# Kernel optimization log

Measured on AMD Instinct MI355X. Metric: run time of the kernel, lower is better.

## Reference

```python
import jax, jax.numpy as jnp
import numpy as np

B, C_IN, C_OUT, T, K, STRIDE, PAD = 16, 256, 256, 4096, 3, 1, 1


def deform_conv1d(x, offset, weight, bias):
    # x: (B,C,T); offset: (B,2K,Tout,1) interleaved (dy,dx); weight: (O,C,K); bias: (O,)
    Bn, C, Tn = x.shape
    O, _, Kn = weight.shape
    dy = offset[:, 0::2, :, 0]  # (B,K,Tout)
    dx = offset[:, 1::2, :, 0]  # (B,K,Tout)
    Tout = dy.shape[-1]
    # offset_mode='center': subtract dcn_base_offset (y base = k-pad, x base = 0)
    base_y = jnp.arange(Kn, dtype=x.dtype) - PAD
    dy = dy - base_y[None, :, None]
    # sampling position along T: t*stride - pad + k + dy
    t0 = jnp.arange(Tout, dtype=x.dtype) * STRIDE - PAD
    py = t0[None, None, :] + jnp.arange(Kn, dtype=x.dtype)[None, :, None] + dy  # (B,K,Tout)
    i0 = jnp.floor(py)
    frac = py - i0
    i0i = i0.astype(jnp.int32)

    def gather(idx):
        valid = ((idx >= 0) & (idx < Tn)).astype(x.dtype)  # zero padding outside
        idxc = jnp.clip(idx, 0, Tn - 1).reshape(Bn, 1, Kn * Tout)
        v = jnp.take_along_axis(x, jnp.broadcast_to(idxc, (Bn, C, Kn * Tout)), axis=2)
        return v.reshape(Bn, C, Kn, Tout) * valid[:, None]

    # linear interp along T
    v = gather(i0i) * (1.0 - frac)[:, None] + gather(i0i + 1) * frac[:, None]  # (B,C,K,Tout)
    # bilinear weight along the dummy width dim (W=1, base x index 0)
    wx = jnp.maximum(0.0, 1.0 - jnp.abs(dx))  # (B,K,Tout)
    v = v * wx[:, None]
    out = jnp.einsum('bckt,ock->bot', v, weight) + bias[None, :, None]
    return out


def setup_inputs() -> dict:
    key = jax.random.key(0)
    k1, k2, k3, k4 = jax.random.split(key, 4)
    x = jax.random.normal(k1, (B, C_IN, T), dtype=jnp.float32)
    offset = jax.random.normal(k2, (B, 2 * K, T, 1), dtype=jnp.float32)
    fan_in = C_IN * K
    bound = 1.0 / np.sqrt(fan_in)
    weight = jax.random.uniform(k3, (C_OUT, C_IN, K), minval=-bound, maxval=bound, dtype=jnp.float32)
    bias = jax.random.uniform(k4, (C_OUT,), minval=-bound, maxval=bound, dtype=jnp.float32)
    return {"x": x, "offset": offset, "weight": weight, "bias": bias}


def reference(x, offset, weight, bias):
    return deform_conv1d(x, offset, weight, bias)
```

## Files before the change

kernel.cpp:

```cpp
#include <hip/hip_runtime.h>
#include <hip/hip_bf16.h>

typedef __attribute__((ext_vector_type(8))) short bf16x8;
typedef __attribute__((ext_vector_type(4))) float f32x4;

constexpr int NB = 16, CIN = 256, COUT = 256, TDIM = 4096, KS = 3, PADV = 1;
constexpr int TT = 64;
constexpr int NSTEP = 12;

typedef __attribute__((address_space(1))) const unsigned int gu32;
typedef __attribute__((address_space(3))) unsigned int lu32;

static __device__ __forceinline__ ushort f2bf(float f) {
    union { __hip_bfloat16 h; ushort u; } cv;
    cv.h = __float2bfloat16(f);
    return cv.u;
}
static __device__ __forceinline__ float bf2f(ushort u) {
    union { unsigned int u32; float f; } cv;
    cv.u32 = ((unsigned int)u) << 16;
    return cv.f;
}

__global__ __launch_bounds__(256) void prepack_w2(const float* __restrict__ w,
                                                  __hip_bfloat16* __restrict__ wp2) {
    int idx = blockIdx.x * 256 + threadIdx.x;
    if (idx >= NSTEP * COUT * 64) return;
    int e    = idx & 7;
    int lane = (idx >> 3) & 63;
    int mf   = (idx >> 9) & 1;
    int kb   = (idx >> 10) & 1;
    int wid  = (idx >> 11) & 3;
    int ot   = (idx >> 13) & 1;
    int s    = idx >> 14;
    int o = ot * 128 + wid * 32 + mf * 16 + (lane & 15);
    int k = s % 3;
    int c = (s / 3) * 64 + kb * 32 + (lane >> 4) * 8 + e;
    wp2[idx] = __float2bfloat16(w[(o * CIN + c) * KS + k]);
}

__global__ __launch_bounds__(256) void prepack_w(const float* __restrict__ w,
                                                 __hip_bfloat16* __restrict__ wp) {
    int idx = blockIdx.x * 256 + threadIdx.x;
    if (idx >= NSTEP * COUT * 64) return;
    int e  = idx & 7;
    int j  = (idx >> 3) & 7;
    int o  = (idx >> 6) & (COUT - 1);
    int s  = idx >> 14;
    int k  = s % 3;
    int c  = (s / 3) * 64 + ((j ^ (o & 7)) << 3) + e;
    wp[idx] = __float2bfloat16(w[(o * CIN + c) * KS + k]);
}

__global__ __launch_bounds__(256) void transpose_x(const float* __restrict__ x,
                                                   ushort* __restrict__ xT) {
    __shared__ ushort tile[64][72];
    const int b  = blockIdx.z;
    const int c0 = blockIdx.y * 64;
    const int t0 = blockIdx.x * 64;
    const int tid = threadIdx.x;
    {
        const int c  = tid >> 2;
        const int tq = (tid & 3) << 4;
        const float* src = x + ((size_t)(b * CIN + c0 + c)) * TDIM + t0 + tq;
        #pragma unroll
        for (int i = 0; i < 4; ++i) {
            float4 f = *(const float4*)(src + 4 * i);
            tile[tq + 4 * i + 0][c] = f2bf(f.x);
            tile[tq + 4 * i + 1][c] = f2bf(f.y);
            tile[tq + 4 * i + 2][c] = f2bf(f.z);
            tile[tq + 4 * i + 3][c] = f2bf(f.w);
        }
    }
    __syncthreads();
    {
        const int t = tid >> 2;
        const int q = tid & 3;
        const uint4* lp = (const uint4*)&tile[t][q * 16];
        uint4 v0 = lp[0], v1 = lp[1];
        uint4* dst = (uint4*)(xT + ((size_t)b * TDIM + t0 + t) * CIN + c0 + q * 16);
        dst[0] = v0;
        dst[1] = v1;
    }
}

__global__ __launch_bounds__(256, 4) void deform_mfma_xt(
    const ushort* __restrict__ xT,
    const float* __restrict__ off,
    const ushort* __restrict__ wp2,
    const float* __restrict__ bias,
    float* __restrict__ out)
{
    __shared__ ushort v_s[TT * 64];
    __shared__ int4   sP[KS][TT];

    const int tid = threadIdx.x;

    const int bid = blockIdx.x;
    const int q   = bid & 7;
    const int r   = bid >> 3;
    const int b   = 2 * q + (r >> 7);
    const int r2  = r & 127;
    const int ot  = r2 >> 6;
    const int tt0 = (r2 & 63) * TT;

    if (tid < KS * TT) {
        int k = tid >> 6, j = tid & (TT - 1);
        int t = tt0 + j;
        float dyr = off[((b * 2 * KS + 2 * k) * TDIM) + t];
        float dxr = off[((b * 2 * KS + 2 * k + 1) * TDIM) + t];
        float dyk = dyr - (float)(k - PADV);
        float py  = (float)(t - PADV + k) + dyk;
        float i0f = floorf(py);
        float fr  = py - i0f;
        int i0 = (int)i0f, i1 = i0 + 1;
        float wx = fmaxf(0.0f, 1.0f - fabsf(dxr));
        float w0 = (1.0f - fr) * wx * ((i0 >= 0 && i0 < TDIM) ? 1.0f : 0.0f);
        float w1 = fr * wx * ((i1 >= 0 && i1 < TDIM) ? 1.0f : 0.0f);
        int base = min(max(i0, 0), TDIM - 2);
        bool iA = (i0 == base);
        float wa = iA ? w0 : ((i0 + 1 == base) ? w1 : 0.0f);
        float wb = iA ? w1 : ((i0 == base + 1) ? w0 : 0.0f);
        int4 p;
        p.x = base;
        p.y = __float_as_int(wa);
        p.z = __float_as_int(wb);
        p.w = 0;
        sP[k][j] = p;
    }

    const int wid  = tid >> 6;
    const int lane = tid & 63;
    const int lr   = lane & 15;
    const int lg   = lane >> 4;

    const int tg   = tid >> 3;
    const int slot = tid & 7;
    const int t0l  = tg;
    const int t1l  = tg + 32;
    const int voffA = (t0l * 128 + slot * 16) ^ ((t0l & 7) << 4);
    const int voffB = (t1l * 128 + slot * 16) ^ ((t1l & 7) << 4);

    f32x4 acc[2][4];
    #pragma unroll
    for (int i = 0; i < 2; ++i)
        #pragma unroll
        for (int j = 0; j < 4; ++j) acc[i][j] = (f32x4)0.0f;

    const ushort* xTb = xT + (size_t)b * TDIM * CIN;

    for (int cb = 0; cb < 4; ++cb) {
      const int cbase = cb * 64;
      for (int k = 0; k < 3; ++k) {
        const int s_idx = cb * 3 + k;
        __syncthreads();

        const ushort* wslot = wp2 + (size_t)(((s_idx * 2 + ot) * 4 + wid) * 4) * 512
                                  + lane * 8;
        bf16x8 af00 = *(const bf16x8*)(wslot);
        bf16x8 af01 = *(const bf16x8*)(wslot + 512);
        bf16x8 af10 = *(const bf16x8*)(wslot + 1024);
        bf16x8 af11 = *(const bf16x8*)(wslot + 1536);

        {
            int4 e0 = sP[k][t0l];
            int4 e1 = sP[k][t1l];
            const ushort* rowA = xTb + (size_t)e0.x * CIN + cbase + slot * 8;
            const ushort* rowB = xTb + (size_t)e1.x * CIN + cbase + slot * 8;
            bf16x8 a0 = *(const bf16x8*)rowA;
            bf16x8 a1 = *(const bf16x8*)(rowA + CIN);
            bf16x8 b0 = *(const bf16x8*)rowB;
            bf16x8 b1 = *(const bf16x8*)(rowB + CIN);
            float wa0 = __int_as_float(e0.y), wb0 = __int_as_float(e0.z);
            float wa1 = __int_as_float(e1.y), wb1 = __int_as_float(e1.z);
            bf16x8 pk0, pk1;
            #pragma unroll
            for (int i = 0; i < 8; ++i) {
                pk0[i] = (short)f2bf(bf2f((ushort)a0[i]) * wa0 + bf2f((ushort)a1[i]) * wb0);
                pk1[i] = (short)f2bf(bf2f((ushort)b0[i]) * wa1 + bf2f((ushort)b1[i]) * wb1);
            }
            *(bf16x8*)((char*)v_s + voffA) = pk0;
            *(bf16x8*)((char*)v_s + voffB) = pk1;
        }

        __syncthreads();

        #pragma unroll
        for (int kb = 0; kb < 2; ++kb) {
            const int kk = kb * 32 + lg * 8;
            bf16x8 bfr[4];
            #pragma unroll
            for (int nf = 0; nf < 4; ++nf) {
                int tc = nf * 16 + lr;
                int byte = (tc * 128 + kk * 2) ^ ((tc & 7) << 4);
                bfr[nf] = *(const bf16x8*)((const char*)v_s + byte);
            }
            bf16x8 a0 = kb ? af10 : af00;
            bf16x8 a1 = kb ? af11 : af01;
            #pragma unroll
            for (int nf = 0; nf < 4; ++nf) {
                acc[0][nf] = __builtin_amdgcn_mfma_f32_16x16x32_bf16(a0, bfr[nf], acc[0][nf], 0, 0, 0);
                acc[1][nf] = __builtin_amdgcn_mfma_f32_16x16x32_bf16(a1, bfr[nf], acc[1][nf], 0, 0, 0);
            }
        }
      }
    }

    #pragma unroll
    for (int mf = 0; mf < 2; ++mf) {
        #pragma unroll
        for (int rg = 0; rg < 4; ++rg) {
            int o = ot * 128 + wid * 32 + mf * 16 + lg * 4 + rg;
            float bv = bias[o];
            float* orow = out + (size_t)(b * COUT + o) * TDIM + tt0;
            #pragma unroll
            for (int nf = 0; nf < 4; ++nf)
                orow[nf * 16 + lr] = acc[mf][nf][rg] + bv;
        }
    }
}

__global__ __launch_bounds__(512, 4) void deform_mfma_gather(
    const float* __restrict__ x,
    const float* __restrict__ off,
    const __hip_bfloat16* __restrict__ wp,
    const float* __restrict__ bias,
    float* __restrict__ out)
{
    __shared__ ushort w_s[COUT * 64];
    __shared__ ushort v_s[128 * 64];
    __shared__ int4   sP[KS][128];

    const int tid = threadIdx.x;
    const int bid  = blockIdx.x;
    const int q    = bid & 7;
    const int r    = bid >> 3;
    const int b    = 2 * q + (r >> 5);
    const int tt0  = (r & 31) * 128;

    if (tid < KS * 128) {
        int k = tid >> 7, j = tid & 127;
        int t = tt0 + j;
        float dyr = off[((b * 2 * KS + 2 * k) * TDIM) + t];
        float dxr = off[((b * 2 * KS + 2 * k + 1) * TDIM) + t];
        float py  = (float)(t - PADV + k) + dyr - (float)(k - PADV);
        float i0f = floorf(py);
        float fr  = py - i0f;
        int i0 = (int)i0f, i1 = i0 + 1;
        float wx = fmaxf(0.0f, 1.0f - fabsf(dxr));
        float w0 = (1.0f - fr) * wx * ((i0 >= 0 && i0 < TDIM) ? 1.0f : 0.0f);
        float w1 = fr * wx * ((i1 >= 0 && i1 < TDIM) ? 1.0f : 0.0f);
        int4 p;
        p.x = min(max(i0, 0), TDIM - 1);
        p.y = min(max(i1, 0), TDIM - 1);
        p.z = __float_as_int(w0);
        p.w = __float_as_int(w1);
        sP[k][j] = p;
    }

    const int wid    = tid >> 6;
    const int lane   = tid & 63;
    const int o_base = (wid >> 1) * 64;
    const int t_base = (wid & 1) * 64;
    const int lr     = lane & 15;
    const int lg     = lane >> 4;

    f32x4 acc[4][4];
    #pragma unroll
    for (int i = 0; i < 4; ++i)
        #pragma unroll
        for (int j = 0; j < 4; ++j) acc[i][j] = (f32x4)0.0f;

    const float* xb = x + (size_t)b * CIN * TDIM;

    for (int cb = 0; cb < 4; ++cb) {
      for (int k = 0; k < 3; ++k) {
        const int s_idx = cb * 3 + k;
        const int c0    = cb * 64;
        __syncthreads();
        {
            const char* gbase = (const char*)wp + (size_t)s_idx * 32768 + wid * 4096 + lane * 16;
            char* lbase = (char*)w_s + wid * 4096;
            #pragma unroll
            for (int i = 0; i < 4; ++i)
                __builtin_amdgcn_global_load_lds((gu32*)(gbase + i * 1024),
                                                 (lu32*)(lbase + i * 1024), 16, 0, 0);
        }
        {
            const int coct0 = tid >> 7;
            const int t     = tid & 127;
            int4 p = sP[k][t];
            const float* xr0 = xb + (size_t)(c0 + coct0 * 8) * TDIM;
            const float* xr1 = xr0 + (size_t)32 * TDIM;
            float g0[16], g1[16];
            #pragma unroll
            for (int i = 0; i < 8; ++i) {
                g0[2 * i]     = xr0[p.x];
                g0[2 * i + 1] = xr0[p.y];
                xr0 += TDIM;
            }
            #pragma unroll
            for (int i = 0; i < 8; ++i) {
                g1[2 * i]     = xr1[p.x];
                g1[2 * i + 1] = xr1[p.y];
                xr1 += TDIM;
            }
            float w0 = __int_as_float(p.z), w1 = __int_as_float(p.w);
            bf16x8 pk0, pk1;
            #pragma unroll
            for (int i = 0; i < 8; ++i) {
                pk0[i] = (short)f2bf(g0[2 * i] * w0 + g0[2 * i + 1] * w1);
                pk1[i] = (short)f2bf(g1[2 * i] * w0 + g1[2 * i + 1] * w1);
            }
            int row = t * 128;
            int swz = (t & 7) << 4;
            *(bf16x8*)((char*)v_s + ((row + coct0 * 16) ^ swz))       = pk0;
            *(bf16x8*)((char*)v_s + ((row + (coct0 + 4) * 16) ^ swz)) = pk1;
        }
        __syncthreads();
        #pragma unroll
        for (int kb = 0; kb < 2; ++kb) {
            const int kk = kb * 32 + lg * 8;
            bf16x8 bfr[4];
            #pragma unroll
            for (int nf = 0; nf < 4; ++nf) {
                int tc = t_base + nf * 16 + lr;
                int byte = (tc * 128 + kk * 2) ^ ((tc & 7) << 4);
                bfr[nf] = *(const bf16x8*)((const char*)v_s + byte);
            }
            #pragma unroll
            for (int mf = 0; mf < 4; ++mf) {
                int o  = o_base + mf * 16 + lr;
                int byte = (o * 128 + kk * 2) ^ ((o & 7) << 4);
                bf16x8 af = *(const bf16x8*)((const char*)w_s + byte);
                #pragma unroll
                for (int nf = 0; nf < 4; ++nf)
                    acc[mf][nf] = __builtin_amdgcn_mfma_f32_16x16x32_bf16(
                        af, bfr[nf], acc[mf][nf], 0, 0, 0);
            }
        }
      }
    }

    #pragma unroll
    for (int mf = 0; mf < 4; ++mf) {
        #pragma unroll
        for (int rg = 0; rg < 4; ++rg) {
            int o = o_base + mf * 16 + lg * 4 + rg;
            float bv = bias[o];
            float* orow = out + (size_t)(b * COUT + o) * TDIM + tt0 + t_base;
            #pragma unroll
            for (int nf = 0; nf < 4; ++nf)
                orow[nf * 16 + lr] = acc[mf][nf][rg] + bv;
        }
    }
}

extern "C" void kernel_launch(void* const* d_in, const int* in_sizes, int n_in,
                              void* d_out, int out_size, void* d_ws, size_t ws_size,
                              hipStream_t stream) {
    const float* x    = (const float*)d_in[0];
    const float* off  = (const float*)d_in[1];
    const float* w    = (const float*)d_in[2];
    const float* bias = (const float*)d_in[3];
    float* out = (float*)d_out;

    const size_t xt_off  = 512 * 1024;
    const size_t xt_need = xt_off + (size_t)NB * TDIM * CIN * sizeof(ushort);

    if (ws_size >= xt_need) {
        ushort* wp2 = (ushort*)d_ws;
        ushort* xT  = (ushort*)((char*)d_ws + xt_off);
        prepack_w2<<<dim3(768), dim3(256), 0, stream>>>(w, (__hip_bfloat16*)wp2);
        transpose_x<<<dim3(TDIM / 64, CIN / 64, NB), dim3(256), 0, stream>>>(x, xT);
        deform_mfma_xt<<<dim3(2048), dim3(256), 0, stream>>>(xT, off, wp2, bias, out);
    } else {
        __hip_bfloat16* wp = (__hip_bfloat16*)d_ws;
        prepack_w<<<dim3(768), dim3(256), 0, stream>>>(w, wp);
        deform_mfma_gather<<<dim3(512), dim3(512), 0, stream>>>(x, off, wp, bias, out);
    }
}
```

Measured before the change: 68.79 us.

## Software-pipeline gather and weight loads one step ahead of MFMA compute

Restructures the 12-step channel/tap loop so the global loads of x rows and weight fragments for step s+1 are issued before the MFMAs of step s, and the interpolation and bf16 packing run after the MFMAs. This hides global-memory latency behind matrix work. Manual s_barrier, sched_barrier and lgkmcnt waits replace __syncthreads to control ordering. In exchange it holds more live registers for the prefetched data and adds one redundant prefetch on the last step.

```diff
diff --git a/kernel.cpp b/kernel.cpp
--- a/kernel.cpp
+++ b/kernel.cpp
@@ -149,41 +149,65 @@
 
     const ushort* xTb = xT + (size_t)b * TDIM * CIN;
 
-    for (int cb = 0; cb < 4; ++cb) {
-      const int cbase = cb * 64;
-      for (int k = 0; k < 3; ++k) {
-        const int s_idx = cb * 3 + k;
-        __syncthreads();
-
-        const ushort* wslot = wp2 + (size_t)(((s_idx * 2 + ot) * 4 + wid) * 4) * 512
-                                  + lane * 8;
-        bf16x8 af00 = *(const bf16x8*)(wslot);
-        bf16x8 af01 = *(const bf16x8*)(wslot + 512);
-        bf16x8 af10 = *(const bf16x8*)(wslot + 1024);
-        bf16x8 af11 = *(const bf16x8*)(wslot + 1536);
-
-        {
-            int4 e0 = sP[k][t0l];
-            int4 e1 = sP[k][t1l];
-            const ushort* rowA = xTb + (size_t)e0.x * CIN + cbase + slot * 8;
-            const ushort* rowB = xTb + (size_t)e1.x * CIN + cbase + slot * 8;
-            bf16x8 a0 = *(const bf16x8*)rowA;
-            bf16x8 a1 = *(const bf16x8*)(rowA + CIN);
-            bf16x8 b0 = *(const bf16x8*)rowB;
-            bf16x8 b1 = *(const bf16x8*)(rowB + CIN);
-            float wa0 = __int_as_float(e0.y), wb0 = __int_as_float(e0.z);
-            float wa1 = __int_as_float(e1.y), wb1 = __int_as_float(e1.z);
-            bf16x8 pk0, pk1;
-            #pragma unroll
-            for (int i = 0; i < 8; ++i) {
-                pk0[i] = (short)f2bf(bf2f((ushort)a0[i]) * wa0 + bf2f((ushort)a1[i]) * wb0);
-                pk1[i] = (short)f2bf(bf2f((ushort)b0[i]) * wa1 + bf2f((ushort)b1[i]) * wb1);
-            }
-            *(bf16x8*)((char*)v_s + voffA) = pk0;
-            *(bf16x8*)((char*)v_s + voffB) = pk1;
-        }
-
-        __syncthreads();
+    __syncthreads();
+
+    bf16x8 af0, af1, af2, af3;
+    bf16x8 pk0, pk1;
+    {
+        const ushort* wslot = wp2 + (size_t)(((0 * 2 + ot) * 4 + wid) * 4) * 512 + lane * 8;
+        af0 = *(const bf16x8*)(wslot);
+        af1 = *(const bf16x8*)(wslot + 512);
+        af2 = *(const bf16x8*)(wslot + 1024);
+        af3 = *(const bf16x8*)(wslot + 1536);
+        int4 e0 = sP[0][t0l];
+        int4 e1 = sP[0][t1l];
+        const ushort* rowA = xTb + (size_t)e0.x * CIN + slot * 8;
+        const ushort* rowB = xTb + (size_t)e1.x * CIN + slot * 8;
+        bf16x8 a0 = *(const bf16x8*)rowA;
+        bf16x8 a1 = *(const bf16x8*)(rowA + CIN);
+        bf16x8 b0 = *(const bf16x8*)rowB;
+        bf16x8 b1 = *(const bf16x8*)(rowB + CIN);
+        float wa0 = __int_as_float(e0.y), wb0 = __int_as_float(e0.z);
+        float wa1 = __int_as_float(e1.y), wb1 = __int_as_float(e1.z);
+        #pragma unroll
+        for (int i = 0; i < 8; ++i) {
+            pk0[i] = (short)f2bf(bf2f((ushort)a0[i]) * wa0 + bf2f((ushort)a1[i]) * wb0);
+            pk1[i] = (short)f2bf(bf2f((ushort)b0[i]) * wa1 + bf2f((ushort)b1[i]) * wb1);
+        }
+    }
+
+    #pragma unroll 1
+    for (int s = 0; s < NSTEP; ++s) {
+        const int sn  = (s + 1 < NSTEP) ? s + 1 : NSTEP - 1;
+        const int kn  = sn % 3;
+        const int cbn = (sn / 3) * 64;
+
+        __builtin_amdgcn_s_barrier();
+        __builtin_amdgcn_sched_barrier(0);
+
+        *(bf16x8*)((char*)v_s + voffA) = pk0;
+        *(bf16x8*)((char*)v_s + voffB) = pk1;
+
+        const ushort* wslot = wp2 + (size_t)(((sn * 2 + ot) * 4 + wid) * 4) * 512 + lane * 8;
+        bf16x8 an0 = *(const bf16x8*)(wslot);
+        bf16x8 an1 = *(const bf16x8*)(wslot + 512);
+        bf16x8 an2 = *(const bf16x8*)(wslot + 1024);
+        bf16x8 an3 = *(const bf16x8*)(wslot + 1536);
+
+        int4 e0 = sP[kn][t0l];
+        int4 e1 = sP[kn][t1l];
+        const ushort* rowA = xTb + (size_t)e0.x * CIN + cbn + slot * 8;
+        const ushort* rowB = xTb + (size_t)e1.x * CIN + cbn + slot * 8;
+        bf16x8 ga0 = *(const bf16x8*)rowA;
+        bf16x8 ga1 = *(const bf16x8*)(rowA + CIN);
+        bf16x8 gb0 = *(const bf16x8*)rowB;
+        bf16x8 gb1 = *(const bf16x8*)(rowB + CIN);
+
+        __builtin_amdgcn_sched_barrier(0);
+        asm volatile("s_waitcnt lgkmcnt(0)" ::: "memory");
+        __builtin_amdgcn_sched_barrier(0);
+        __builtin_amdgcn_s_barrier();
+        __builtin_amdgcn_sched_barrier(0);
 
         #pragma unroll
         for (int kb = 0; kb < 2; ++kb) {
@@ -195,15 +219,26 @@
                 int byte = (tc * 128 + kk * 2) ^ ((tc & 7) << 4);
                 bfr[nf] = *(const bf16x8*)((const char*)v_s + byte);
             }
-            bf16x8 a0 = kb ? af10 : af00;
-            bf16x8 a1 = kb ? af11 : af01;
+            bf16x8 a0 = kb ? af2 : af0;
+            bf16x8 a1 = kb ? af3 : af1;
             #pragma unroll
             for (int nf = 0; nf < 4; ++nf) {
                 acc[0][nf] = __builtin_amdgcn_mfma_f32_16x16x32_bf16(a0, bfr[nf], acc[0][nf], 0, 0, 0);
                 acc[1][nf] = __builtin_amdgcn_mfma_f32_16x16x32_bf16(a1, bfr[nf], acc[1][nf], 0, 0, 0);
             }
         }
-      }
+        __builtin_amdgcn_sched_barrier(0);
+
+        {
+            float wa0 = __int_as_float(e0.y), wb0 = __int_as_float(e0.z);
+            float wa1 = __int_as_float(e1.y), wb1 = __int_as_float(e1.z);
+            #pragma unroll
+            for (int i = 0; i < 8; ++i) {
+                pk0[i] = (short)f2bf(bf2f((ushort)ga0[i]) * wa0 + bf2f((ushort)ga1[i]) * wb0);
+                pk1[i] = (short)f2bf(bf2f((ushort)gb0[i]) * wa1 + bf2f((ushort)gb1[i]) * wb1);
+            }
+        }
+        af0 = an0; af1 = an1; af2 = an2; af3 = an3;
     }
 
     #pragma unroll
```

Result: slower. 70.86 us (+3.0%).
